# Kernel tuning notes

Measured on AMD Instinct MI355X. Metric: run time of the kernel, lower is better.

The kernel has to match this reference:

```python
import jax, jax.numpy as jnp
import numpy as np

K = 16          # nsample / knn k
GROUPS = 4      # GroupNorm groups
EPS = 1e-5


def setup_inputs() -> dict:
    key = jax.random.key(0)
    ks = jax.random.split(key, 10)
    B, N = 8, 2048
    x = jax.random.normal(ks[0], (B, 3, N), jnp.float32)
    f = x  # at first call features == coordinates
    w = lambda i, shape: jax.random.normal(ks[i], shape, jnp.float32) * 0.05
    return dict(
        x=x, f=f,
        # input_trans: Conv1d(3 -> 64)
        W_it=w(1, (64, 3)), b_it=jnp.zeros((64,), jnp.float32),
        # layer1: Conv2d(128 -> 128, bias=False) + GroupNorm(4, 128)
        W1=w(2, (128, 128)), gn_g=jnp.ones((128,), jnp.float32), gn_b=jnp.zeros((128,), jnp.float32),
        # mlp1: Conv2d(128->256), Conv2d(256->512)
        Wa=w(3, (256, 128)), ba=jnp.zeros((256,), jnp.float32),
        Wb=w(4, (512, 256)), bb=jnp.zeros((512,), jnp.float32),
        # mlp2: Conv1d(640->256), Conv1d(256->128)
        Wc=w(5, (256, 640)), bc=jnp.zeros((256,), jnp.float32),
        Wd=w(6, (128, 256)), bd=jnp.zeros((128,), jnp.float32),
        # mlp3: Conv1d(128->256), Conv1d(256->512)
        We=w(7, (256, 128)), be=jnp.zeros((256,), jnp.float32),
        Wf=w(8, (512, 256)), bf=jnp.zeros((512,), jnp.float32),
    )


def _knn_idx(x):
    # x: (B, 3, N) -> idx: (B, N, K) indices of K nearest neighbors (self-knn)
    coor = jnp.transpose(x, (0, 2, 1))                       # (B, N, 3)
    sq = jnp.sum(coor * coor, axis=-1)                        # (B, N)
    d = sq[:, :, None] + sq[:, None, :] - 2.0 * jnp.einsum('bnc,bmc->bnm', coor, coor)
    _, idx = jax.lax.top_k(-d, K)                             # smallest distances
    return idx


def _group_norm(y, gamma, beta):
    # y: (B, N, K, C); torch GroupNorm normalizes over (C/g, N, K) per (b, group)
    B, N, Kk, C = y.shape
    yg = y.reshape(B, N, Kk, GROUPS, C // GROUPS)
    mu = jnp.mean(yg, axis=(1, 2, 4), keepdims=True)
    var = jnp.var(yg, axis=(1, 2, 4), keepdims=True)
    yg = (yg - mu) * jax.lax.rsqrt(var + EPS)
    return yg.reshape(B, N, Kk, C) * gamma + beta


def reference(x, f, W_it, b_it, W1, gn_g, gn_b, Wa, ba, Wb, bb, Wc, bc, Wd, bd, We, be, Wf, bf):
    B, _, N = x.shape
    idx = _knn_idx(x)                                          # (B, N, K)

    # input_trans: 1x1 conv over channels, channels-last layout (B, N, C)
    h = jnp.einsum('bcn,oc->bno', f, W_it) + b_it              # (B, N, 64)

    # graph feature: gather neighbors, build [nb - h, h]
    nb = jax.vmap(lambda hb, ib: hb[ib])(h, idx)               # (B, N, K, 64)
    hq = h[:, :, None, :]                                       # (B, N, 1, 64)
    feat = jnp.concatenate([nb - hq, jnp.broadcast_to(hq, nb.shape)], axis=-1)  # (B, N, K, 128)

    # layer1: conv1x1 (no bias) + GroupNorm + LeakyReLU(0.2)
    y = jnp.einsum('bnkc,oc->bnko', feat, W1)                  # (B, N, K, 128)
    y = jax.nn.leaky_relu(_group_norm(y, gn_g, gn_b), 0.2)

    local_base = jnp.max(y, axis=2)                             # (B, N, 128)

    # mlp1 over edges, then max over K and global max over N
    g = jax.nn.relu(jnp.einsum('bnkc,oc->bnko', y, Wa) + ba)    # (B, N, K, 256)
    g = jax.nn.relu(jnp.einsum('bnkc,oc->bnko', g, Wb) + bb)    # (B, N, K, 512)
    gfeat = jnp.max(g, axis=2)                                  # (B, N, 512)
    gmax = jnp.max(gfeat, axis=1, keepdims=True)                # (B, 1, 512)

    cat = jnp.concatenate([local_base, jnp.broadcast_to(gmax, (B, N, 512))], axis=-1)  # (B, N, 640)

    lf = jax.nn.relu(jnp.einsum('bnc,oc->bno', cat, Wc) + bc)   # (B, N, 256)
    lf = jax.nn.relu(jnp.einsum('bnc,oc->bno', lf, Wd) + bd)    # (B, N, 128)

    gl = jax.nn.relu(jnp.einsum('bnc,oc->bno', lf, We) + be)    # (B, N, 256)
    gl = jax.nn.relu(jnp.einsum('bnc,oc->bno', gl, Wf) + bf)    # (B, N, 512)
    gl = jnp.max(gl, axis=1, keepdims=True)                     # (B, 1, 512)

    global_feat = jnp.transpose(gl, (0, 2, 1))                  # (B, 512, 1)
    local_feat = jnp.transpose(lf, (0, 2, 1))                   # (B, 128, N)
    return (global_feat, local_feat)
```

## Files before the change

kernel.cpp:

```cpp
#include <hip/hip_runtime.h>

#define BATCH 8
#define NPTS 2048
#define KNNK 16
#define CH 64
#define CF 128
#define CA 256
#define CB 512
#define CCAT 640
#define CC 256
#define CD 128
#define CE 256
#define CG 512
#define NGRP 4
#define EPSF 1e-5f
#define GF_OFF (BATCH*CG)
#define P 8
#define MROWS (P*KNNK)
#define TM 64

typedef __attribute__((ext_vector_type(8))) short short8v;
typedef __attribute__((ext_vector_type(4))) float f32x4;

__device__ inline short f2bf(float f) {
  union { float f; unsigned u; } v; v.f = f;
  unsigned r = v.u + 0x7fff + ((v.u >> 16) & 1);
  return (short)(r >> 16);
}

#define LIDX(r, c, ROW) ((r)*(ROW) + ((c) ^ (((r)&7)<<3)))

__global__ void k_transpose(const float* __restrict__ src, float* __restrict__ dst,
                            int R, int C) {
  int i = blockIdx.x * 256 + threadIdx.x;
  if (i < R * C) {
    int r = i / C, c = i - r * C;
    dst[c * R + r] = src[i];
  }
}

__global__ void k_pack(const float* __restrict__ W, short* __restrict__ Wp,
                       int O, int C, int ld) {
  int tid = blockIdx.x * 256 + threadIdx.x;
  int KS = C >> 5;
  int total = (O >> 4) * KS * 64;
  if (tid >= total) return;
  int l = tid & 63;
  int fs = tid >> 6;
  int nt = fs / KS, ks = fs - nt * KS;
  int o = nt * 16 + (l & 15);
  int c = ks * 32 + (l >> 4) * 8;
  const float* src = W + (size_t)o * ld + c;
  short8v v;
#pragma unroll
  for (int j = 0; j < 8; ++j) v[j] = f2bf(src[j]);
  *(short8v*)&Wp[(size_t)tid * 8] = v;
}

__global__ void k_sq_h(const float* __restrict__ x, const float* __restrict__ f,
                       const float* __restrict__ Wit, const float* __restrict__ bit,
                       float* __restrict__ h) {
  int t = blockIdx.x * 256 + threadIdx.x;
  if (t >= BATCH * NPTS * CH) return;
  int o = t & (CH - 1);
  int bn = t >> 6;
  int n = bn & (NPTS - 1);
  int b = bn >> 11;
  float f0 = f[(b*3 + 0)*NPTS + n];
  float f1 = f[(b*3 + 1)*NPTS + n];
  float f2 = f[(b*3 + 2)*NPTS + n];
  h[t] = f0*Wit[o*3+0] + f1*Wit[o*3+1] + f2*Wit[o*3+2] + bit[o];
}

__global__ __launch_bounds__(256)
void k_knn(const float* __restrict__ x, int* __restrict__ idxout) {
  __shared__ float xs0[2112], xs1[2112], xs2[2112], sqs[2112];
  int blk = blockIdx.x;
  int b = blk >> 9;
  int n0 = (blk & 511) * 4;
  int t = threadIdx.x;
  for (int i = t; i < NPTS; i += 256) {
    float x0 = x[(b*3 + 0)*NPTS + i];
    float x1 = x[(b*3 + 1)*NPTS + i];
    float x2 = x[(b*3 + 2)*NPTS + i];
    int a = (i >> 5)*33 + (i & 31);
    xs0[a] = x0; xs1[a] = x1; xs2[a] = x2;
    sqs[a] = __fadd_rn(__fadd_rn(__fmul_rn(x0,x0), __fmul_rn(x1,x1)), __fmul_rn(x2,x2));
  }
  __syncthreads();
  int lane = t & 63, wv = t >> 6;
  int q = n0 + wv;
  int qa = (q >> 5)*33 + (q & 31);
  float qx = xs0[qa], qy = xs1[qa], qz = xs2[qa];
  float sqq = sqs[qa];
  float d[32];
  int base = lane * 32;
#pragma unroll
  for (int jj = 0; jj < 32; ++jj) {
    int a = lane*33 + jj;
    float mx = xs0[a], my = xs1[a], mz = xs2[a];
    float dot = __fadd_rn(__fadd_rn(__fmul_rn(qx,mx), __fmul_rn(qy,my)), __fmul_rn(qz,mz));
    d[jj] = __fsub_rn(__fadd_rn(sqq, sqs[a]), __fadd_rn(dot, dot));
  }
  const float FINF = __builtin_inff();
  float sv0 = d[0]; int si0 = base;
#pragma unroll
  for (int jj = 1; jj < 16; ++jj)
    if (d[jj] < sv0) { sv0 = d[jj]; si0 = base + jj; }
  float sv1 = d[16]; int si1 = base + 16;
#pragma unroll
  for (int jj = 17; jj < 32; ++jj)
    if (d[jj] < sv1) { sv1 = d[jj]; si1 = base + jj; }
  int gsel = 0;
#pragma unroll
  for (int r = 0; r < KNNK; ++r) {
    float v = sv0; int i = si0;
    if (sv1 < v || (sv1 == v && si1 < i)) { v = sv1; i = si1; }
#pragma unroll
    for (int off = 32; off > 0; off >>= 1) {
      float v2 = __shfl_xor(v, off);
      int   i2 = __shfl_xor(i, off);
      if (v2 < v || (v2 == v && i2 < i)) { v = v2; i = i2; }
    }
    if (lane == r) gsel = i;
    int rem = ((i >> 5) == lane) ? (i & 31) : 64;
    if (rem < 16) {
      float nv = FINF; int ni = 0x7fffffff;
#pragma unroll
      for (int jj = 0; jj < 16; ++jj) {
        float dv = (jj == rem) ? FINF : d[jj];
        d[jj] = dv;
        if (dv < nv) { nv = dv; ni = base + jj; }
      }
      sv0 = nv; si0 = ni;
    } else if (rem < 32) {
      float nv = FINF; int ni = 0x7fffffff;
#pragma unroll
      for (int jj = 16; jj < 32; ++jj) {
        float dv = (jj == rem) ? FINF : d[jj];
        d[jj] = dv;
        if (dv < nv) { nv = dv; ni = base + jj; }
      }
      sv1 = nv; si1 = ni;
    }
  }
  if (lane < KNNK) idxout[(size_t)(b*NPTS + q)*KNNK + lane] = gsel;
}

__device__ inline void stage_feat(short* featS, const float* __restrict__ h,
                                  const int* __restrict__ idx, int b, int n0, int t) {
  int r = t >> 1, cb = (t & 1) * 32;
  int p = r >> 4, kk = r & 15;
  int nbi = idx[(size_t)(b*NPTS + n0 + p)*KNNK + kk];
  const float* hq = h + (size_t)(b*NPTS + n0 + p)*CH;
  const float* hn = h + (size_t)(b*NPTS + nbi)*CH;
#pragma unroll
  for (int j = 0; j < 32; j += 8) {
    float4 q0 = *(const float4*)(hq + cb + j);
    float4 q1 = *(const float4*)(hq + cb + j + 4);
    float4 a0 = *(const float4*)(hn + cb + j);
    float4 a1 = *(const float4*)(hn + cb + j + 4);
    short8v dv, qv;
    dv[0]=f2bf(a0.x-q0.x); dv[1]=f2bf(a0.y-q0.y); dv[2]=f2bf(a0.z-q0.z); dv[3]=f2bf(a0.w-q0.w);
    dv[4]=f2bf(a1.x-q1.x); dv[5]=f2bf(a1.y-q1.y); dv[6]=f2bf(a1.z-q1.z); dv[7]=f2bf(a1.w-q1.w);
    qv[0]=f2bf(q0.x); qv[1]=f2bf(q0.y); qv[2]=f2bf(q0.z); qv[3]=f2bf(q0.w);
    qv[4]=f2bf(q1.x); qv[5]=f2bf(q1.y); qv[6]=f2bf(q1.z); qv[7]=f2bf(q1.w);
    *(short8v*)&featS[LIDX(r, cb + j, CF)] = dv;
    *(short8v*)&featS[LIDX(r, 64 + cb + j, CF)] = qv;
  }
}

__global__ __launch_bounds__(256, 2)
void k_stats(const float* __restrict__ h, const int* __restrict__ idx,
             const short* __restrict__ W1p, float* __restrict__ partials) {
  __shared__ short featS[MROWS*CF];
  int blk = blockIdx.x;
  int b = blk >> 8;
  int n0 = (blk & 255) * P;
  int t = threadIdx.x;
  stage_feat(featS, h, idx, b, n0, t);
  __syncthreads();
  int lane = t & 63, wv = t >> 6;
  int r16 = lane & 15, g8 = (lane >> 4) * 8;
  short8v af[8][4];
#pragma unroll
  for (int m = 0; m < 8; ++m)
#pragma unroll
    for (int ks = 0; ks < 4; ++ks)
      af[m][ks] = *(const short8v*)&featS[LIDX(m*16 + r16, ks*32 + g8, CF)];
  float s = 0.f, ss = 0.f;
#pragma unroll
  for (int n = 0; n < 2; ++n) {
    int nt = 2*wv + n;
    short8v bfr[4];
#pragma unroll
    for (int ks = 0; ks < 4; ++ks)
      bfr[ks] = *(const short8v*)&W1p[(size_t)((nt*4 + ks)*64 + lane)*8];
#pragma unroll
    for (int m = 0; m < 8; ++m) {
      f32x4 acc = {0.f, 0.f, 0.f, 0.f};
#pragma unroll
      for (int ks = 0; ks < 4; ++ks)
        acc = __builtin_amdgcn_mfma_f32_16x16x32_bf16(af[m][ks], bfr[ks], acc, 0, 0, 0);
#pragma unroll
      for (int i = 0; i < 4; ++i) { s += acc[i]; ss += acc[i]*acc[i]; }
    }
  }
#pragma unroll
  for (int off = 32; off > 0; off >>= 1) {
    s += __shfl_xor(s, off);
    ss += __shfl_xor(ss, off);
  }
  if (lane == 0) {
    partials[(size_t)(blk*NGRP + wv)*2 + 0] = s;
    partials[(size_t)(blk*NGRP + wv)*2 + 1] = ss;
  }
}

__global__ void k_reduce(const float* __restrict__ partials, float* __restrict__ stats) {
  int b = blockIdx.x >> 2, g = blockIdx.x & 3;
  int t = threadIdx.x;
  float s  = partials[(size_t)((b*256 + t)*NGRP + g)*2 + 0];
  float ss = partials[(size_t)((b*256 + t)*NGRP + g)*2 + 1];
  __shared__ float rs[256], rss[256];
  rs[t] = s; rss[t] = ss;
  __syncthreads();
  for (int st = 128; st > 0; st >>= 1) {
    if (t < st) { rs[t] += rs[t+st]; rss[t] += rss[t+st]; }
    __syncthreads();
  }
  if (t == 0) {
    const float cnt = (float)((size_t)NPTS * KNNK * 32);
    float mu = rs[0] / cnt;
    float var = rss[0] / cnt - mu*mu;
    stats[(b*NGRP+g)*2+0] = mu;
    stats[(b*NGRP+g)*2+1] = rsqrtf(var + EPSF);
  }
}

__global__ __launch_bounds__(256, 2)
void k_main(const float* __restrict__ h, const int* __restrict__ idx,
            const short* __restrict__ W1p, const float* __restrict__ gng,
            const float* __restrict__ gnb, const float* __restrict__ stats,
            const short* __restrict__ Wap, const float* __restrict__ ba,
            const short* __restrict__ Wbp, const float* __restrict__ bb,
            float* __restrict__ lbase, unsigned* __restrict__ gmaxU) {
  __shared__ short lds[MROWS*CA];
  short* featS = lds;
  short* ynS   = lds + MROWS*CF;
  short* g1S   = lds;
  int blk = blockIdx.x;
  int b = blk >> 8;
  int n0 = (blk & 255) * P;
  int t = threadIdx.x;
  stage_feat(featS, h, idx, b, n0, t);
  __syncthreads();
  int lane = t & 63, wv = t >> 6;
  int r16 = lane & 15, g8 = (lane >> 4) * 8;
  int rowg = (lane >> 4) * 4;
  {
    short8v af[8][4];
#pragma unroll
    for (int m = 0; m < 8; ++m)
#pragma unroll
      for (int ks = 0; ks < 4; ++ks)
        af[m][ks] = *(const short8v*)&featS[LIDX(m*16 + r16, ks*32 + g8, CF)];
    float mu  = stats[(b*NGRP + wv)*2 + 0];
    float rsg = stats[(b*NGRP + wv)*2 + 1];
#pragma unroll
    for (int n = 0; n < 2; ++n) {
      int nt = 2*wv + n;
      int o = nt*16 + r16;
      short8v bfr[4];
#pragma unroll
      for (int ks = 0; ks < 4; ++ks)
        bfr[ks] = *(const short8v*)&W1p[(size_t)((nt*4 + ks)*64 + lane)*8];
      float ga = gng[o], bev = gnb[o];
#pragma unroll
      for (int m = 0; m < 8; ++m) {
        f32x4 acc = {0.f, 0.f, 0.f, 0.f};
#pragma unroll
        for (int ks = 0; ks < 4; ++ks)
          acc = __builtin_amdgcn_mfma_f32_16x16x32_bf16(af[m][ks], bfr[ks], acc, 0, 0, 0);
        float vmax = -3.0e38f;
#pragma unroll
        for (int i = 0; i < 4; ++i) {
          float v = (acc[i] - mu) * rsg * ga + bev;
          v = (v >= 0.f) ? v : 0.2f*v;
          vmax = fmaxf(vmax, v);
          ynS[LIDX(m*16 + rowg + i, o, CF)] = f2bf(v);
        }
        vmax = fmaxf(vmax, __shfl_xor(vmax, 16));
        vmax = fmaxf(vmax, __shfl_xor(vmax, 32));
        if (lane < 16) lbase[(size_t)(b*NPTS + n0 + m)*CF + o] = vmax;
      }
    }
  }
  __syncthreads();
  {
    short8v yf[8][4];
#pragma unroll
    for (int m = 0; m < 8; ++m)
#pragma unroll
      for (int ks = 0; ks < 4; ++ks)
        yf[m][ks] = *(const short8v*)&ynS[LIDX(m*16 + r16, ks*32 + g8, CF)];
    __syncthreads();
#pragma unroll
    for (int nn = 0; nn < 4; ++nn) {
      int nt = wv*4 + nn;
      int o = nt*16 + r16;
      short8v bfr[4];
#pragma unroll
      for (int ks = 0; ks < 4; ++ks)
        bfr[ks] = *(const short8v*)&Wap[(size_t)((nt*4 + ks)*64 + lane)*8];
      float bav = ba[o];
#pragma unroll
      for (int m = 0; m < 8; ++m) {
        f32x4 acc = {0.f, 0.f, 0.f, 0.f};
#pragma unroll
        for (int ks = 0; ks < 4; ++ks)
          acc = __builtin_amdgcn_mfma_f32_16x16x32_bf16(yf[m][ks], bfr[ks], acc, 0, 0, 0);
#pragma unroll
        for (int i = 0; i < 4; ++i) {
          float v = fmaxf(acc[i] + bav, 0.f);
          g1S[LIDX(m*16 + rowg + i, o, CA)] = f2bf(v);
        }
      }
    }
  }
  __syncthreads();
#pragma unroll
  for (int half = 0; half < 2; ++half) {
    f32x4 acc[4][8];
#pragma unroll
    for (int nn = 0; nn < 4; ++nn)
#pragma unroll
      for (int m = 0; m < 8; ++m) acc[nn][m] = (f32x4){0.f, 0.f, 0.f, 0.f};
#pragma unroll
    for (int ks = 0; ks < 8; ++ks) {
      short8v gfk[8];
#pragma unroll
      for (int m = 0; m < 8; ++m)
        gfk[m] = *(const short8v*)&g1S[LIDX(m*16 + r16, ks*32 + g8, CA)];
#pragma unroll
      for (int nn = 0; nn < 4; ++nn) {
        int nt = wv*8 + half*4 + nn;
        short8v bfr = *(const short8v*)&Wbp[(size_t)((nt*8 + ks)*64 + lane)*8];
#pragma unroll
        for (int m = 0; m < 8; ++m)
          acc[nn][m] = __builtin_amdgcn_mfma_f32_16x16x32_bf16(gfk[m], bfr, acc[nn][m], 0, 0, 0);
      }
    }
#pragma unroll
    for (int nn = 0; nn < 4; ++nn) {
      int nt = wv*8 + half*4 + nn;
      float b0 = bb[nt*16 + r16];
      float am = 0.f;
#pragma unroll
      for (int m = 0; m < 8; ++m)
#pragma unroll
        for (int i = 0; i < 4; ++i) am = fmaxf(am, acc[nn][m][i] + b0);
      am = fmaxf(am, __shfl_xor(am, 16));
      am = fmaxf(am, __shfl_xor(am, 32));
      if (lane < 16) atomicMax(&gmaxU[b*CG + nt*16 + lane], __float_as_uint(am));
    }
  }
}

__global__ void k_gbias(const unsigned* __restrict__ gmaxU, const float* __restrict__ WcT,
                        const float* __restrict__ bc, float* __restrict__ bceff) {
  int b = blockIdx.x;
  int o = threadIdx.x;
  float acc = bc[o];
  for (int c = 0; c < CB; ++c)
    acc += __uint_as_float(gmaxU[b*CG + c]) * WcT[(size_t)(CF + c)*CC + o];
  bceff[b*CC + o] = acc;
}

__global__ __launch_bounds__(256)
void k_tail(const float* __restrict__ lbase, const float* __restrict__ bceff,
            const short* __restrict__ WcLp,
            const short* __restrict__ Wdp, const float* __restrict__ bd,
            const short* __restrict__ Wep, const float* __restrict__ be,
            const short* __restrict__ Wfp, const float* __restrict__ bf,
            float* __restrict__ out, unsigned* __restrict__ glmaxU) {
  __shared__ short aS0[TM*CF];
  __shared__ short aS1[TM*CA];
  int blk = blockIdx.x;
  int b = blk >> 5;
  int n0 = (blk & 31) * TM;
  int t = threadIdx.x;
  {
    int r = t >> 2, cb = (t & 3) * 32;
    const float* src = lbase + (size_t)(b*NPTS + n0 + r)*CF + cb;
#pragma unroll
    for (int j = 0; j < 32; j += 8) {
      float4 v0 = *(const float4*)(src + j);
      float4 v1 = *(const float4*)(src + j + 4);
      short8v pv;
      pv[0]=f2bf(v0.x); pv[1]=f2bf(v0.y); pv[2]=f2bf(v0.z); pv[3]=f2bf(v0.w);
      pv[4]=f2bf(v1.x); pv[5]=f2bf(v1.y); pv[6]=f2bf(v1.z); pv[7]=f2bf(v1.w);
      *(short8v*)&aS0[LIDX(r, cb + j, CF)] = pv;
    }
  }
  __syncthreads();
  int lane = t & 63, wv = t >> 6;
  int r16 = lane & 15, g8 = (lane >> 4) * 8;
  int rowg = (lane >> 4) * 4;
  {
    short8v af[4][4];
#pragma unroll
    for (int mt = 0; mt < 4; ++mt)
#pragma unroll
      for (int ks = 0; ks < 4; ++ks)
        af[mt][ks] = *(const short8v*)&aS0[LIDX(mt*16 + r16, ks*32 + g8, CF)];
#pragma unroll
    for (int nn = 0; nn < 4; ++nn) {
      int nt = wv*4 + nn;
      int o = nt*16 + r16;
      short8v bfr[4];
#pragma unroll
      for (int ks = 0; ks < 4; ++ks)
        bfr[ks] = *(const short8v*)&WcLp[(size_t)((nt*4 + ks)*64 + lane)*8];
      float bce = bceff[b*CC + o];
#pragma unroll
      for (int mt = 0; mt < 4; ++mt) {
        f32x4 acc = {0.f, 0.f, 0.f, 0.f};
#pragma unroll
        for (int ks = 0; ks < 4; ++ks)
          acc = __builtin_amdgcn_mfma_f32_16x16x32_bf16(af[mt][ks], bfr[ks], acc, 0, 0, 0);
#pragma unroll
        for (int i = 0; i < 4; ++i)
          aS1[LIDX(mt*16 + rowg + i, o, CA)] = f2bf(fmaxf(acc[i] + bce, 0.f));
      }
    }
  }
  __syncthreads();
  {
    short8v af[4][8];
#pragma unroll
    for (int mt = 0; mt < 4; ++mt)
#pragma unroll
      for (int ks = 0; ks < 8; ++ks)
        af[mt][ks] = *(const short8v*)&aS1[LIDX(mt*16 + r16, ks*32 + g8, CA)];
#pragma unroll
    for (int nn = 0; nn < 2; ++nn) {
      int nt = wv*2 + nn;
      int o = nt*16 + r16;
      short8v bfr[8];
#pragma unroll
      for (int ks = 0; ks < 8; ++ks)
        bfr[ks] = *(const short8v*)&Wdp[(size_t)((nt*8 + ks)*64 + lane)*8];
      float bdv = bd[o];
#pragma unroll
      for (int mt = 0; mt < 4; ++mt) {
        f32x4 acc = {0.f, 0.f, 0.f, 0.f};
#pragma unroll
        for (int ks = 0; ks < 8; ++ks)
          acc = __builtin_amdgcn_mfma_f32_16x16x32_bf16(af[mt][ks], bfr[ks], acc, 0, 0, 0);
#pragma unroll
        for (int i = 0; i < 4; ++i) {
          float v = fmaxf(acc[i] + bdv, 0.f);
          aS0[LIDX(mt*16 + rowg + i, o, CF)] = f2bf(v);
          out[GF_OFF + ((size_t)(b*CD + o))*NPTS + n0 + mt*16 + rowg + i] = v;
        }
      }
    }
  }
  __syncthreads();
  {
    short8v af[4][4];
#pragma unroll
    for (int mt = 0; mt < 4; ++mt)
#pragma unroll
      for (int ks = 0; ks < 4; ++ks)
        af[mt][ks] = *(const short8v*)&aS0[LIDX(mt*16 + r16, ks*32 + g8, CF)];
#pragma unroll
    for (int nn = 0; nn < 4; ++nn) {
      int nt = wv*4 + nn;
      int o = nt*16 + r16;
      short8v bfr[4];
#pragma unroll
      for (int ks = 0; ks < 4; ++ks)
        bfr[ks] = *(const short8v*)&Wep[(size_t)((nt*4 + ks)*64 + lane)*8];
      float bev = be[o];
#pragma unroll
      for (int mt = 0; mt < 4; ++mt) {
        f32x4 acc = {0.f, 0.f, 0.f, 0.f};
#pragma unroll
        for (int ks = 0; ks < 4; ++ks)
          acc = __builtin_amdgcn_mfma_f32_16x16x32_bf16(af[mt][ks], bfr[ks], acc, 0, 0, 0);
#pragma unroll
        for (int i = 0; i < 4; ++i)
          aS1[LIDX(mt*16 + rowg + i, o, CA)] = f2bf(fmaxf(acc[i] + bev, 0.f));
      }
    }
  }
  __syncthreads();
  {
    short8v af[4][8];
#pragma unroll
    for (int mt = 0; mt < 4; ++mt)
#pragma unroll
      for (int ks = 0; ks < 8; ++ks)
        af[mt][ks] = *(const short8v*)&aS1[LIDX(mt*16 + r16, ks*32 + g8, CA)];
#pragma unroll
    for (int nn = 0; nn < 8; ++nn) {
      int nt = wv*8 + nn;
      short8v bfr[8];
#pragma unroll
      for (int ks = 0; ks < 8; ++ks)
        bfr[ks] = *(const short8v*)&Wfp[(size_t)((nt*8 + ks)*64 + lane)*8];
      float bfv = bf[nt*16 + r16];
      float am = 0.f;
#pragma unroll
      for (int mt = 0; mt < 4; ++mt) {
        f32x4 acc = {0.f, 0.f, 0.f, 0.f};
#pragma unroll
        for (int ks = 0; ks < 8; ++ks)
          acc = __builtin_amdgcn_mfma_f32_16x16x32_bf16(af[mt][ks], bfr[ks], acc, 0, 0, 0);
#pragma unroll
        for (int i = 0; i < 4; ++i) am = fmaxf(am, acc[i] + bfv);
      }
      am = fmaxf(am, __shfl_xor(am, 16));
      am = fmaxf(am, __shfl_xor(am, 32));
      if (lane < 16) atomicMax(&glmaxU[b*CG + nt*16 + lane], __float_as_uint(am));
    }
  }
}

__global__ void k_final(const unsigned* __restrict__ glmaxU, float* __restrict__ out) {
  int i = blockIdx.x*256 + threadIdx.x;
  if (i < BATCH*CG) out[i] = __uint_as_float(glmaxU[i]);
}

extern "C" void kernel_launch(void* const* d_in, const int* in_sizes, int n_in,
                              void* d_out, int out_size, void* d_ws, size_t ws_size,
                              hipStream_t stream) {
  const float* x   = (const float*)d_in[0];
  const float* f   = (const float*)d_in[1];
  const float* Wit = (const float*)d_in[2];
  const float* bit = (const float*)d_in[3];
  const float* W1  = (const float*)d_in[4];
  const float* gng = (const float*)d_in[5];
  const float* gnb = (const float*)d_in[6];
  const float* Wa  = (const float*)d_in[7];
  const float* ba  = (const float*)d_in[8];
  const float* Wb  = (const float*)d_in[9];
  const float* bb  = (const float*)d_in[10];
  const float* Wc  = (const float*)d_in[11];
  const float* bc  = (const float*)d_in[12];
  const float* Wd  = (const float*)d_in[13];
  const float* bd  = (const float*)d_in[14];
  const float* We  = (const float*)d_in[15];
  const float* be  = (const float*)d_in[16];
  const float* Wf  = (const float*)d_in[17];
  const float* bf  = (const float*)d_in[18];
  float* out = (float*)d_out;

  char* w = (char*)d_ws;
  size_t off = 0;
  auto alloc = [&](size_t bytes) {
    void* p = w + off; off += (bytes + 255) & ~(size_t)255; return p;
  };
  float* h        = (float*)alloc((size_t)BATCH*NPTS*CH*4);
  int*   idx      = (int*)  alloc((size_t)BATCH*NPTS*KNNK*4);
  short* W1p      = (short*)alloc((size_t)CF*CF*2);
  short* Wap      = (short*)alloc((size_t)CA*CF*2);
  short* Wbp      = (short*)alloc((size_t)CB*CA*2);
  short* WcLp     = (short*)alloc((size_t)CC*CF*2);
  short* Wdp      = (short*)alloc((size_t)CD*CC*2);
  short* Wep      = (short*)alloc((size_t)CE*CD*2);
  short* Wfp      = (short*)alloc((size_t)CG*CE*2);
  float* WcT      = (float*)alloc((size_t)CCAT*CC*4);
  float* bceff    = (float*)alloc((size_t)BATCH*CC*4);
  float* partials = (float*)alloc((size_t)(BATCH*NPTS/P)*NGRP*2*4);
  float* stats    = (float*)alloc((size_t)BATCH*NGRP*2*4);
  float* lbase    = (float*)alloc((size_t)BATCH*NPTS*CF*4);
  unsigned* gmaxU  = (unsigned*)alloc((size_t)BATCH*CG*4);
  unsigned* glmaxU = (unsigned*)alloc((size_t)BATCH*CG*4);

  hipMemsetAsync(gmaxU, 0, (size_t)BATCH*CG*4, stream);
  hipMemsetAsync(glmaxU, 0, (size_t)BATCH*CG*4, stream);

  k_pack<<<8,  256, 0, stream>>>(W1, W1p, CF, CF, CF);
  k_pack<<<16, 256, 0, stream>>>(Wa, Wap, CA, CF, CF);
  k_pack<<<64, 256, 0, stream>>>(Wb, Wbp, CB, CA, CA);
  k_pack<<<16, 256, 0, stream>>>(Wc, WcLp, CC, CF, CCAT);
  k_pack<<<16, 256, 0, stream>>>(Wd, Wdp, CD, CC, CC);
  k_pack<<<16, 256, 0, stream>>>(We, Wep, CE, CD, CD);
  k_pack<<<64, 256, 0, stream>>>(Wf, Wfp, CG, CE, CE);
  k_transpose<<<(CC*CCAT+255)/256, 256, 0, stream>>>(Wc, WcT, CC, CCAT);

  k_sq_h<<<(BATCH*NPTS*CH+255)/256, 256, 0, stream>>>(x, f, Wit, bit, h);
  k_knn<<<BATCH*NPTS/4, 256, 0, stream>>>(x, idx);
  k_stats<<<BATCH*NPTS/P, 256, 0, stream>>>(h, idx, W1p, partials);
  k_reduce<<<BATCH*NGRP, 256, 0, stream>>>(partials, stats);
  k_main<<<BATCH*NPTS/P, 256, 0, stream>>>(h, idx, W1p, gng, gnb, stats,
                                           Wap, ba, Wbp, bb, lbase, gmaxU);
  k_gbias<<<BATCH, 256, 0, stream>>>(gmaxU, WcT, bc, bceff);
  k_tail<<<BATCH*NPTS/TM, 256, 0, stream>>>(lbase, bceff, WcLp, Wdp, bd,
                                            Wep, be, Wfp, bf, out, glmaxU);
  k_final<<<(BATCH*CG+255)/256, 256, 0, stream>>>(glmaxU, out);
}
```

Measured before the change: 300.8 us.

## Fuse prep kernels, swap MFMA operands, widen KNN blocks, drop Wc transpose

Merges the seven weight-pack launches and the input transform into one k_prep kernel, and removes the Wc transpose by having k_gbias read Wc directly with a wave-level shuffle reduction. All MFMA calls swap their A/B operands so each lane holds four consecutive output channels. That lets epilogues load bias and GroupNorm parameters as float4, write packed short4 values to LDS, and do the max reductions with 16-lane shuffles. The k_main mlp1b loop is re-tiled to 8 N-tiles by 4 M-tiles per half. KNN moves to 512-thread blocks covering 8 queries. The launch-count and vectorisation gains come with more register pressure and changed global store patterns, for example the strided local_feat writes.

Result: slower. 461.3 us (+53.4%).

```diff
diff --git a/kernel.cpp b/kernel.cpp
--- a/kernel.cpp
+++ b/kernel.cpp
@@ -20,6 +20,7 @@
 #define TM 64
 
 typedef __attribute__((ext_vector_type(8))) short short8v;
+typedef __attribute__((ext_vector_type(4))) short short4v;
 typedef __attribute__((ext_vector_type(4))) float f32x4;
 
 __device__ inline short f2bf(float f) {
@@ -30,18 +31,8 @@
 
 #define LIDX(r, c, ROW) ((r)*(ROW) + ((c) ^ (((r)&7)<<3)))
 
-__global__ void k_transpose(const float* __restrict__ src, float* __restrict__ dst,
-                            int R, int C) {
-  int i = blockIdx.x * 256 + threadIdx.x;
-  if (i < R * C) {
-    int r = i / C, c = i - r * C;
-    dst[c * R + r] = src[i];
-  }
-}
-
-__global__ void k_pack(const float* __restrict__ W, short* __restrict__ Wp,
-                       int O, int C, int ld) {
-  int tid = blockIdx.x * 256 + threadIdx.x;
+__device__ inline void pack_dev(const float* __restrict__ W, short* __restrict__ Wp,
+                                int O, int C, int ld, int tid) {
   int KS = C >> 5;
   int total = (O >> 4) * KS * 64;
   if (tid >= total) return;
@@ -57,29 +48,44 @@
   *(short8v*)&Wp[(size_t)tid * 8] = v;
 }
 
-__global__ void k_sq_h(const float* __restrict__ x, const float* __restrict__ f,
-                       const float* __restrict__ Wit, const float* __restrict__ bit,
-                       float* __restrict__ h) {
-  int t = blockIdx.x * 256 + threadIdx.x;
-  if (t >= BATCH * NPTS * CH) return;
-  int o = t & (CH - 1);
-  int bn = t >> 6;
-  int n = bn & (NPTS - 1);
-  int b = bn >> 11;
-  float f0 = f[(b*3 + 0)*NPTS + n];
-  float f1 = f[(b*3 + 1)*NPTS + n];
-  float f2 = f[(b*3 + 2)*NPTS + n];
-  h[t] = f0*Wit[o*3+0] + f1*Wit[o*3+1] + f2*Wit[o*3+2] + bit[o];
-}
-
 __global__ __launch_bounds__(256)
+void k_prep(const float* __restrict__ f, const float* __restrict__ Wit,
+            const float* __restrict__ bit, float* __restrict__ h,
+            const float* __restrict__ W1, short* __restrict__ W1p,
+            const float* __restrict__ Wa, short* __restrict__ Wap,
+            const float* __restrict__ Wb, short* __restrict__ Wbp,
+            const float* __restrict__ Wc, short* __restrict__ WcLp,
+            const float* __restrict__ Wd, short* __restrict__ Wdp,
+            const float* __restrict__ We, short* __restrict__ Wep,
+            const float* __restrict__ Wf, short* __restrict__ Wfp) {
+  int blk = blockIdx.x;
+  if (blk < 4096) {
+    int t = blk * 256 + threadIdx.x;
+    int o = t & (CH - 1);
+    int bn = t >> 6;
+    int n = bn & (NPTS - 1);
+    int b = bn >> 11;
+    float f0 = f[(b*3 + 0)*NPTS + n];
+    float f1 = f[(b*3 + 1)*NPTS + n];
+    float f2 = f[(b*3 + 2)*NPTS + n];
+    h[t] = f0*Wit[o*3+0] + f1*Wit[o*3+1] + f2*Wit[o*3+2] + bit[o];
+  } else if (blk < 4104) pack_dev(W1, W1p, CF, CF, CF, (blk-4096)*256 + threadIdx.x);
+  else if (blk < 4120) pack_dev(Wa, Wap, CA, CF, CF, (blk-4104)*256 + threadIdx.x);
+  else if (blk < 4184) pack_dev(Wb, Wbp, CB, CA, CA, (blk-4120)*256 + threadIdx.x);
+  else if (blk < 4200) pack_dev(Wc, WcLp, CC, CF, CCAT, (blk-4184)*256 + threadIdx.x);
+  else if (blk < 4216) pack_dev(Wd, Wdp, CD, CC, CC, (blk-4200)*256 + threadIdx.x);
+  else if (blk < 4232) pack_dev(We, Wep, CE, CD, CD, (blk-4216)*256 + threadIdx.x);
+  else                 pack_dev(Wf, Wfp, CG, CE, CE, (blk-4232)*256 + threadIdx.x);
+}
+
+__global__ __launch_bounds__(512)
 void k_knn(const float* __restrict__ x, int* __restrict__ idxout) {
   __shared__ float xs0[2112], xs1[2112], xs2[2112], sqs[2112];
   int blk = blockIdx.x;
-  int b = blk >> 9;
-  int n0 = (blk & 511) * 4;
+  int b = blk >> 8;
+  int n0 = (blk & 255) * 8;
   int t = threadIdx.x;
-  for (int i = t; i < NPTS; i += 256) {
+  for (int i = t; i < NPTS; i += 512) {
     float x0 = x[(b*3 + 0)*NPTS + i];
     float x1 = x[(b*3 + 1)*NPTS + i];
     float x2 = x[(b*3 + 2)*NPTS + i];
@@ -256,7 +262,7 @@
   stage_feat(featS, h, idx, b, n0, t);
   __syncthreads();
   int lane = t & 63, wv = t >> 6;
-  int r16 = lane & 15, g8 = (lane >> 4) * 8;
+  int kk = lane & 15, g8 = (lane >> 4) * 8;
   int rowg = (lane >> 4) * 4;
   {
     short8v af[8][4];
@@ -264,35 +270,43 @@
     for (int m = 0; m < 8; ++m)
 #pragma unroll
       for (int ks = 0; ks < 4; ++ks)
-        af[m][ks] = *(const short8v*)&featS[LIDX(m*16 + r16, ks*32 + g8, CF)];
+        af[m][ks] = *(const short8v*)&featS[LIDX(m*16 + kk, ks*32 + g8, CF)];
     float mu  = stats[(b*NGRP + wv)*2 + 0];
     float rsg = stats[(b*NGRP + wv)*2 + 1];
 #pragma unroll
     for (int n = 0; n < 2; ++n) {
       int nt = 2*wv + n;
-      int o = nt*16 + r16;
+      int o4 = nt*16 + rowg;
       short8v bfr[4];
 #pragma unroll
       for (int ks = 0; ks < 4; ++ks)
         bfr[ks] = *(const short8v*)&W1p[(size_t)((nt*4 + ks)*64 + lane)*8];
-      float ga = gng[o], bev = gnb[o];
+      f32x4 ga4 = *(const f32x4*)&gng[o4];
+      f32x4 gb4 = *(const f32x4*)&gnb[o4];
 #pragma unroll
       for (int m = 0; m < 8; ++m) {
         f32x4 acc = {0.f, 0.f, 0.f, 0.f};
 #pragma unroll
         for (int ks = 0; ks < 4; ++ks)
-          acc = __builtin_amdgcn_mfma_f32_16x16x32_bf16(af[m][ks], bfr[ks], acc, 0, 0, 0);
-        float vmax = -3.0e38f;
+          acc = __builtin_amdgcn_mfma_f32_16x16x32_bf16(bfr[ks], af[m][ks], acc, 0, 0, 0);
+        float vm[4];
+        short4v pk;
 #pragma unroll
         for (int i = 0; i < 4; ++i) {
-          float v = (acc[i] - mu) * rsg * ga + bev;
+          float v = (acc[i] - mu) * rsg * ga4[i] + gb4[i];
           v = (v >= 0.f) ? v : 0.2f*v;
-          vmax = fmaxf(vmax, v);
-          ynS[LIDX(m*16 + rowg + i, o, CF)] = f2bf(v);
+          vm[i] = v;
+          pk[i] = f2bf(v);
         }
-        vmax = fmaxf(vmax, __shfl_xor(vmax, 16));
-        vmax = fmaxf(vmax, __shfl_xor(vmax, 32));
-        if (lane < 16) lbase[(size_t)(b*NPTS + n0 + m)*CF + o] = vmax;
+        *(short4v*)&ynS[LIDX(m*16 + kk, o4, CF)] = pk;
+#pragma unroll
+        for (int off = 1; off <= 8; off <<= 1)
+#pragma unroll
+          for (int i = 0; i < 4; ++i) vm[i] = fmaxf(vm[i], __shfl_xor(vm[i], off));
+        if (kk == 0) {
+          f32x4 vm4 = {vm[0], vm[1], vm[2], vm[3]};
+          *(f32x4*)&lbase[(size_t)(b*NPTS + n0 + m)*CF + o4] = vm4;
+        }
       }
     }
   }
@@ -303,81 +317,97 @@
     for (int m = 0; m < 8; ++m)
 #pragma unroll
       for (int ks = 0; ks < 4; ++ks)
-        yf[m][ks] = *(const short8v*)&ynS[LIDX(m*16 + r16, ks*32 + g8, CF)];
+        yf[m][ks] = *(const short8v*)&ynS[LIDX(m*16 + kk, ks*32 + g8, CF)];
     __syncthreads();
 #pragma unroll
     for (int nn = 0; nn < 4; ++nn) {
       int nt = wv*4 + nn;
-      int o = nt*16 + r16;
+      int o4 = nt*16 + rowg;
       short8v bfr[4];
 #pragma unroll
       for (int ks = 0; ks < 4; ++ks)
         bfr[ks] = *(const short8v*)&Wap[(size_t)((nt*4 + ks)*64 + lane)*8];
-      float bav = ba[o];
+      f32x4 ba4 = *(const f32x4*)&ba[o4];
 #pragma unroll
       for (int m = 0; m < 8; ++m) {
         f32x4 acc = {0.f, 0.f, 0.f, 0.f};
 #pragma unroll
         for (int ks = 0; ks < 4; ++ks)
-          acc = __builtin_amdgcn_mfma_f32_16x16x32_bf16(yf[m][ks], bfr[ks], acc, 0, 0, 0);
-#pragma unroll
-        for (int i = 0; i < 4; ++i) {
-          float v = fmaxf(acc[i] + bav, 0.f);
-          g1S[LIDX(m*16 + rowg + i, o, CA)] = f2bf(v);
-        }
-      }
-    }
-  }
-  __syncthreads();
-#pragma unroll
-  for (int half = 0; half < 2; ++half) {
-    f32x4 acc[4][8];
-#pragma unroll
-    for (int nn = 0; nn < 4; ++nn)
-#pragma unroll
-      for (int m = 0; m < 8; ++m) acc[nn][m] = (f32x4){0.f, 0.f, 0.f, 0.f};
+          acc = __builtin_amdgcn_mfma_f32_16x16x32_bf16(bfr[ks], yf[m][ks], acc, 0, 0, 0);
+        short4v pk;
+#pragma unroll
+        for (int i = 0; i < 4; ++i) pk[i] = f2bf(fmaxf(acc[i] + ba4[i], 0.f));
+        *(short4v*)&g1S[LIDX(m*16 + kk, o4, CA)] = pk;
+      }
+    }
+  }
+  __syncthreads();
+#pragma unroll
+  for (int mh = 0; mh < 2; ++mh) {
+    f32x4 acc[8][4];
+#pragma unroll
+    for (int nn = 0; nn < 8; ++nn)
+#pragma unroll
+      for (int mm = 0; mm < 4; ++mm) acc[nn][mm] = (f32x4){0.f, 0.f, 0.f, 0.f};
 #pragma unroll
     for (int ks = 0; ks < 8; ++ks) {
-      short8v gfk[8];
-#pragma unroll
-      for (int m = 0; m < 8; ++m)
-        gfk[m] = *(const short8v*)&g1S[LIDX(m*16 + r16, ks*32 + g8, CA)];
-#pragma unroll
-      for (int nn = 0; nn < 4; ++nn) {
-        int nt = wv*8 + half*4 + nn;
+      short8v gfk[4];
+#pragma unroll
+      for (int mm = 0; mm < 4; ++mm)
+        gfk[mm] = *(const short8v*)&g1S[LIDX((mh*4+mm)*16 + kk, ks*32 + g8, CA)];
+#pragma unroll
+      for (int nn = 0; nn < 8; ++nn) {
+        int nt = wv*8 + nn;
         short8v bfr = *(const short8v*)&Wbp[(size_t)((nt*8 + ks)*64 + lane)*8];
 #pragma unroll
-        for (int m = 0; m < 8; ++m)
-          acc[nn][m] = __builtin_amdgcn_mfma_f32_16x16x32_bf16(gfk[m], bfr, acc[nn][m], 0, 0, 0);
-      }
-    }
-#pragma unroll
-    for (int nn = 0; nn < 4; ++nn) {
-      int nt = wv*8 + half*4 + nn;
-      float b0 = bb[nt*16 + r16];
-      float am = 0.f;
-#pragma unroll
-      for (int m = 0; m < 8; ++m)
-#pragma unroll
-        for (int i = 0; i < 4; ++i) am = fmaxf(am, acc[nn][m][i] + b0);
-      am = fmaxf(am, __shfl_xor(am, 16));
-      am = fmaxf(am, __shfl_xor(am, 32));
-      if (lane < 16) atomicMax(&gmaxU[b*CG + nt*16 + lane], __float_as_uint(am));
-    }
-  }
-}
-
-__global__ void k_gbias(const unsigned* __restrict__ gmaxU, const float* __restrict__ WcT,
-                        const float* __restrict__ bc, float* __restrict__ bceff) {
+        for (int mm = 0; mm < 4; ++mm)
+          acc[nn][mm] = __builtin_amdgcn_mfma_f32_16x16x32_bf16(bfr, gfk[mm], acc[nn][mm], 0, 0, 0);
+      }
+    }
+#pragma unroll
+    for (int nn = 0; nn < 8; ++nn) {
+      int nt = wv*8 + nn;
+      int o4 = nt*16 + rowg;
+      f32x4 bb4 = *(const f32x4*)&bb[o4];
+      float am[4];
+#pragma unroll
+      for (int i = 0; i < 4; ++i) {
+        am[i] = 0.f;
+#pragma unroll
+        for (int mm = 0; mm < 4; ++mm) am[i] = fmaxf(am[i], acc[nn][mm][i] + bb4[i]);
+      }
+#pragma unroll
+      for (int off = 1; off <= 8; off <<= 1)
+#pragma unroll
+        for (int i = 0; i < 4; ++i) am[i] = fmaxf(am[i], __shfl_xor(am[i], off));
+      if (kk == 0) {
+#pragma unroll
+        for (int i = 0; i < 4; ++i)
+          atomicMax(&gmaxU[b*CG + o4 + i], __float_as_uint(am[i]));
+      }
+    }
+  }
+}
+
+__global__ __launch_bounds__(256)
+void k_gbias(const unsigned* __restrict__ gmaxU, const float* __restrict__ Wc,
+             const float* __restrict__ bc, float* __restrict__ bceff) {
+  __shared__ float gs[CB];
   int b = blockIdx.x;
-  int o = threadIdx.x;
-  float acc = bc[o];
-  for (int c = 0; c < CB; ++c)
-    acc += __uint_as_float(gmaxU[b*CG + c]) * WcT[(size_t)(CF + c)*CC + o];
-  bceff[b*CC + o] = acc;
-}
-
-__global__ __launch_bounds__(256)
+  int t = threadIdx.x;
+  int lane = t & 63, wv = t >> 6;
+  for (int i = t; i < CB; i += 256) gs[i] = __uint_as_float(gmaxU[b*CG + i]);
+  __syncthreads();
+  for (int o = wv; o < CC; o += 4) {
+    float acc = 0.f;
+    for (int c = lane; c < CB; c += 64) acc += gs[c] * Wc[(size_t)o*CCAT + CF + c];
+#pragma unroll
+    for (int off = 32; off > 0; off >>= 1) acc += __shfl_xor(acc, off);
+    if (lane == 0) bceff[b*CC + o] = bc[o] + acc;
+  }
+}
+
+__global__ __launch_bounds__(256, 2)
 void k_tail(const float* __restrict__ lbase, const float* __restrict__ bceff,
             const short* __restrict__ WcLp,
             const short* __restrict__ Wdp, const float* __restrict__ bd,
@@ -405,7 +435,7 @@
   }
   __syncthreads();
   int lane = t & 63, wv = t >> 6;
-  int r16 = lane & 15, g8 = (lane >> 4) * 8;
+  int kk = lane & 15, g8 = (lane >> 4) * 8;
   int rowg = (lane >> 4) * 4;
   {
     short8v af[4][4];
@@ -413,25 +443,26 @@
     for (int mt = 0; mt < 4; ++mt)
 #pragma unroll
       for (int ks = 0; ks < 4; ++ks)
-        af[mt][ks] = *(const short8v*)&aS0[LIDX(mt*16 + r16, ks*32 + g8, CF)];
+        af[mt][ks] = *(const short8v*)&aS0[LIDX(mt*16 + kk, ks*32 + g8, CF)];
 #pragma unroll
     for (int nn = 0; nn < 4; ++nn) {
       int nt = wv*4 + nn;
-      int o = nt*16 + r16;
+      int o4 = nt*16 + rowg;
       short8v bfr[4];
 #pragma unroll
       for (int ks = 0; ks < 4; ++ks)
         bfr[ks] = *(const short8v*)&WcLp[(size_t)((nt*4 + ks)*64 + lane)*8];
-      float bce = bceff[b*CC + o];
+      f32x4 bc4 = *(const f32x4*)&bceff[b*CC + o4];
 #pragma unroll
       for (int mt = 0; mt < 4; ++mt) {
         f32x4 acc = {0.f, 0.f, 0.f, 0.f};
 #pragma unroll
         for (int ks = 0; ks < 4; ++ks)
-          acc = __builtin_amdgcn_mfma_f32_16x16x32_bf16(af[mt][ks], bfr[ks], acc, 0, 0, 0);
-#pragma unroll
-        for (int i = 0; i < 4; ++i)
-          aS1[LIDX(mt*16 + rowg + i, o, CA)] = f2bf(fmaxf(acc[i] + bce, 0.f));
+          acc = __builtin_amdgcn_mfma_f32_16x16x32_bf16(bfr[ks], af[mt][ks], acc, 0, 0, 0);
+        short4v pk;
+#pragma unroll
+        for (int i = 0; i < 4; ++i) pk[i] = f2bf(fmaxf(acc[i] + bc4[i], 0.f));
+        *(short4v*)&aS1[LIDX(mt*16 + kk, o4, CA)] = pk;
       }
     }
   }
@@ -442,28 +473,30 @@
     for (int mt = 0; mt < 4; ++mt)
 #pragma unroll
       for (int ks = 0; ks < 8; ++ks)
-        af[mt][ks] = *(const short8v*)&aS1[LIDX(mt*16 + r16, ks*32 + g8, CA)];
+        af[mt][ks] = *(const short8v*)&aS1[LIDX(mt*16 + kk, ks*32 + g8, CA)];
 #pragma unroll
     for (int nn = 0; nn < 2; ++nn) {
       int nt = wv*2 + nn;
-      int o = nt*16 + r16;
+      int o4 = nt*16 + rowg;
       short8v bfr[8];
 #pragma unroll
       for (int ks = 0; ks < 8; ++ks)
         bfr[ks] = *(const short8v*)&Wdp[(size_t)((nt*8 + ks)*64 + lane)*8];
-      float bdv = bd[o];
+      f32x4 bd4 = *(const f32x4*)&bd[o4];
 #pragma unroll
       for (int mt = 0; mt < 4; ++mt) {
         f32x4 acc = {0.f, 0.f, 0.f, 0.f};
 #pragma unroll
         for (int ks = 0; ks < 8; ++ks)
-          acc = __builtin_amdgcn_mfma_f32_16x16x32_bf16(af[mt][ks], bfr[ks], acc, 0, 0, 0);
+          acc = __builtin_amdgcn_mfma_f32_16x16x32_bf16(bfr[ks], af[mt][ks], acc, 0, 0, 0);
+        short4v pk;
 #pragma unroll
         for (int i = 0; i < 4; ++i) {
-          float v = fmaxf(acc[i] + bdv, 0.f);
-          aS0[LIDX(mt*16 + rowg + i, o, CF)] = f2bf(v);
-          out[GF_OFF + ((size_t)(b*CD + o))*NPTS + n0 + mt*16 + rowg + i] = v;
+          float v = fmaxf(acc[i] + bd4[i], 0.f);
+          pk[i] = f2bf(v);
+          out[GF_OFF + (size_t)(b*CD + o4 + i)*NPTS + n0 + mt*16 + kk] = v;
         }
+        *(short4v*)&aS0[LIDX(mt*16 + kk, o4, CF)] = pk;
       }
     }
   }
@@ -474,25 +507,26 @@
     for (int mt = 0; mt < 4; ++mt)
 #pragma unroll
       for (int ks = 0; ks < 4; ++ks)
-        af[mt][ks] = *(const short8v*)&aS0[LIDX(mt*16 + r16, ks*32 + g8, CF)];
+        af[mt][ks] = *(const short8v*)&aS0[LIDX(mt*16 + kk, ks*32 + g8, CF)];
 #pragma unroll
     for (int nn = 0; nn < 4; ++nn) {
       int nt = wv*4 + nn;
-      int o = nt*16 + r16;
+      int o4 = nt*16 + rowg;
       short8v bfr[4];
 #pragma unroll
       for (int ks = 0; ks < 4; ++ks)
         bfr[ks] = *(const short8v*)&Wep[(size_t)((nt*4 + ks)*64 + lane)*8];
-      float bev = be[o];
+      f32x4 be4 = *(const f32x4*)&be[o4];
 #pragma unroll
       for (int mt = 0; mt < 4; ++mt) {
         f32x4 acc = {0.f, 0.f, 0.f, 0.f};
 #pragma unroll
         for (int ks = 0; ks < 4; ++ks)
-          acc = __builtin_amdgcn_mfma_f32_16x16x32_bf16(af[mt][ks], bfr[ks], acc, 0, 0, 0);
-#pragma unroll
-        for (int i = 0; i < 4; ++i)
-          aS1[LIDX(mt*16 + rowg + i, o, CA)] = f2bf(fmaxf(acc[i] + bev, 0.f));
+          acc = __builtin_amdgcn_mfma_f32_16x16x32_bf16(bfr[ks], af[mt][ks], acc, 0, 0, 0);
+        short4v pk;
+#pragma unroll
+        for (int i = 0; i < 4; ++i) pk[i] = f2bf(fmaxf(acc[i] + be4[i], 0.f));
+        *(short4v*)&aS1[LIDX(mt*16 + kk, o4, CA)] = pk;
       }
     }
   }
@@ -503,28 +537,37 @@
     for (int mt = 0; mt < 4; ++mt)
 #pragma unroll
       for (int ks = 0; ks < 8; ++ks)
-        af[mt][ks] = *(const short8v*)&aS1[LIDX(mt*16 + r16, ks*32 + g8, CA)];
+        af[mt][ks] = *(const short8v*)&aS1[LIDX(mt*16 + kk, ks*32 + g8, CA)];
 #pragma unroll
     for (int nn = 0; nn < 8; ++nn) {
       int nt = wv*8 + nn;
+      int o4 = nt*16 + rowg;
       short8v bfr[8];
 #pragma unroll
       for (int ks = 0; ks < 8; ++ks)
         bfr[ks] = *(const short8v*)&Wfp[(size_t)((nt*8 + ks)*64 + lane)*8];
-      float bfv = bf[nt*16 + r16];
-      float am = 0.f;
+      f32x4 bf4 = *(const f32x4*)&bf[o4];
+      float am[4];
+#pragma unroll
+      for (int i = 0; i < 4; ++i) am[i] = 0.f;
 #pragma unroll
       for (int mt = 0; mt < 4; ++mt) {
         f32x4 acc = {0.f, 0.f, 0.f, 0.f};
 #pragma unroll
         for (int ks = 0; ks < 8; ++ks)
-          acc = __builtin_amdgcn_mfma_f32_16x16x32_bf16(af[mt][ks], bfr[ks], acc, 0, 0, 0);
-#pragma unroll
-        for (int i = 0; i < 4; ++i) am = fmaxf(am, acc[i] + bfv);
-      }
-      am = fmaxf(am, __shfl_xor(am, 16));
-      am = fmaxf(am, __shfl_xor(am, 32));
-      if (lane < 16) atomicMax(&glmaxU[b*CG + nt*16 + lane], __float_as_uint(am));
+          acc = __builtin_amdgcn_mfma_f32_16x16x32_bf16(bfr[ks], af[mt][ks], acc, 0, 0, 0);
+#pragma unroll
+        for (int i = 0; i < 4; ++i) am[i] = fmaxf(am[i], acc[i] + bf4[i]);
+      }
+#pragma unroll
+      for (int off = 1; off <= 8; off <<= 1)
+#pragma unroll
+        for (int i = 0; i < 4; ++i) am[i] = fmaxf(am[i], __shfl_xor(am[i], off));
+      if (kk == 0) {
+#pragma unroll
+        for (int i = 0; i < 4; ++i)
+          atomicMax(&glmaxU[b*CG + o4 + i], __float_as_uint(am[i]));
+      }
     }
   }
 }
@@ -572,7 +615,6 @@
   short* Wdp      = (short*)alloc((size_t)CD*CC*2);
   short* Wep      = (short*)alloc((size_t)CE*CD*2);
   short* Wfp      = (short*)alloc((size_t)CG*CE*2);
-  float* WcT      = (float*)alloc((size_t)CCAT*CC*4);
   float* bceff    = (float*)alloc((size_t)BATCH*CC*4);
   float* partials = (float*)alloc((size_t)(BATCH*NPTS/P)*NGRP*2*4);
   float* stats    = (float*)alloc((size_t)BATCH*NGRP*2*4);
@@ -583,22 +625,14 @@
   hipMemsetAsync(gmaxU, 0, (size_t)BATCH*CG*4, stream);
   hipMemsetAsync(glmaxU, 0, (size_t)BATCH*CG*4, stream);
 
-  k_pack<<<8,  256, 0, stream>>>(W1, W1p, CF, CF, CF);
-  k_pack<<<16, 256, 0, stream>>>(Wa, Wap, CA, CF, CF);
-  k_pack<<<64, 256, 0, stream>>>(Wb, Wbp, CB, CA, CA);
-  k_pack<<<16, 256, 0, stream>>>(Wc, WcLp, CC, CF, CCAT);
-  k_pack<<<16, 256, 0, stream>>>(Wd, Wdp, CD, CC, CC);
-  k_pack<<<16, 256, 0, stream>>>(We, Wep, CE, CD, CD);
-  k_pack<<<64, 256, 0, stream>>>(Wf, Wfp, CG, CE, CE);
-  k_transpose<<<(CC*CCAT+255)/256, 256, 0, stream>>>(Wc, WcT, CC, CCAT);
-
-  k_sq_h<<<(BATCH*NPTS*CH+255)/256, 256, 0, stream>>>(x, f, Wit, bit, h);
-  k_knn<<<BATCH*NPTS/4, 256, 0, stream>>>(x, idx);
+  k_prep<<<4296, 256, 0, stream>>>(f, Wit, bit, h, W1, W1p, Wa, Wap, Wb, Wbp,
+                                   Wc, WcLp, Wd, Wdp, We, Wep, Wf, Wfp);
+  k_knn<<<BATCH*NPTS/8, 512, 0, stream>>>(x, idx);
   k_stats<<<BATCH*NPTS/P, 256, 0, stream>>>(h, idx, W1p, partials);
   k_reduce<<<BATCH*NGRP, 256, 0, stream>>>(partials, stats);
   k_main<<<BATCH*NPTS/P, 256, 0, stream>>>(h, idx, W1p, gng, gnb, stats,
                                            Wap, ba, Wbp, bb, lbase, gmaxU);
-  k_gbias<<<BATCH, 256, 0, stream>>>(gmaxU, WcT, bc, bceff);
+  k_gbias<<<BATCH, 256, 0, stream>>>(gmaxU, Wc, bc, bceff);
   k_tail<<<BATCH*NPTS/TM, 256, 0, stream>>>(lbase, bceff, WcLp, Wdp, bd,
                                             Wep, be, Wfp, bf, out, glmaxU);
   k_final<<<(BATCH*CG+255)/256, 256, 0, stream>>>(glmaxU, out);
```
